# Kernel optimization log

Hardware: AMD Instinct MI355X
Metric: run time of the kernel (lower is better)

Reference implementation:

```python
import jax, jax.numpy as jnp
import numpy as np

B, S, D = 4, 4096, 1024
DFF = 4 * D
ACTIVE = 1024  # ceil(S * 0.25)


def setup_inputs() -> dict:
    key = jax.random.key(0)
    ks = jax.random.split(key, 4)
    x = jax.random.normal(ks[0], (B, S, D), dtype=jnp.float32)
    rw = jax.random.normal(ks[1], (D,), dtype=jnp.float32) * 0.02
    rb = jnp.zeros((1,), dtype=jnp.float32)
    w1 = jax.random.normal(ks[2], (D, DFF), dtype=jnp.float32) * 0.02
    b1 = jnp.zeros((DFF,), dtype=jnp.float32)
    w2 = jax.random.normal(ks[3], (DFF, D), dtype=jnp.float32) * 0.02
    b2 = jnp.zeros((D,), dtype=jnp.float32)
    return {"x": x, "rw": rw, "rb": rb, "w1": w1, "b1": b1,
            "w2": w2, "b2": b2, "active_tokens": ACTIVE}


def reference(x, rw, rb, w1, b1, w2, b2, active_tokens):
    b, s, d = x.shape
    # router: Linear(n_embd, 1) -> [B, S] scores
    scores = jnp.einsum('bsd,d->bs', x, rw) + rb[0]
    # top-k tokens per batch row
    _, idx = jax.lax.top_k(scores, active_tokens)          # [B, K] int32
    sel = jnp.take_along_axis(x, idx[..., None], axis=1)   # [B, K, D]
    # dense MLP on selected tokens (exact GELU as in torch nn.GELU)
    h = jax.nn.gelu(jnp.einsum('bkd,df->bkf', sel, w1) + b1, approximate=False)
    out = jnp.einsum('bkf,fd->bkd', h, w2) + b2            # [B, K, D]
    # sigmoid gate from router scores of selected tokens
    gates = jax.nn.sigmoid(jnp.take_along_axis(scores, idx, axis=1))  # [B, K]
    out = out * gates[..., None]
    # scatter back into zeros at selected positions
    flat_idx = (idx + jnp.arange(b, dtype=idx.dtype)[:, None] * s).reshape(-1)
    flat_out = jnp.zeros((b * s, d), dtype=out.dtype)
    flat_out = flat_out.at[flat_idx].set(out.reshape(-1, d))
    return flat_out.reshape(b, s, d)
```

## Files before the change

### kernel.cpp

```cpp
#include <hip/hip_runtime.h>
#include <hip/hip_bf16.h>
#include <cstdint>
#include <cstddef>

#define Bz 4
#define Sz 4096
#define Dz 1024
#define DFFz 4096
#define KACT 1024

typedef __bf16 bf16;
typedef __attribute__((ext_vector_type(8))) __bf16 bf16x8;
typedef __attribute__((ext_vector_type(4))) __bf16 bf16x4;
typedef __attribute__((ext_vector_type(4))) float f32x4;

__device__ __forceinline__ void async16(const void* g, void* l) {
  __builtin_amdgcn_global_load_lds(
      (const __attribute__((address_space(1))) void*)g,
      (__attribute__((address_space(3))) void*)l, 16, 0, 0);
}

__global__ __launch_bounds__(256) void prep_k(const float* __restrict__ x,
                                              const float* __restrict__ rw,
                                              const float* __restrict__ rb,
                                              float* __restrict__ scores,
                                              float4* __restrict__ out4,
                                              const float* __restrict__ w1,
                                              bf16* __restrict__ w1T,
                                              const float* __restrict__ w2,
                                              bf16* __restrict__ w2T) {
  __shared__ float t[32][33];
  const int bid = blockIdx.x;
  const int tid = threadIdx.x;
  if (bid < 4096) {
    int row = bid * 4 + (tid >> 6);
    int lane = tid & 63;
    const float4* xr = (const float4*)(x + (size_t)row * Dz);
    const float4* wr = (const float4*)rw;
    float acc = 0.f;
#pragma unroll
    for (int i = 0; i < 4; ++i) {
      float4 a = xr[lane + i * 64];
      float4 w = wr[lane + i * 64];
      acc += a.x * w.x + a.y * w.y + a.z * w.z + a.w * w.w;
    }
#pragma unroll
    for (int d = 32; d; d >>= 1) acc += __shfl_down(acc, d, 64);
    if (lane == 0) scores[row] = acc + rb[0];
    float4* o = out4 + (size_t)bid * 4 * (Dz / 4);
    const float4 z = make_float4(0.f, 0.f, 0.f, 0.f);
#pragma unroll
    for (int i = 0; i < 4; ++i) o[tid + i * 256] = z;
  } else {
    const float* in; bf16* outp; int R, C, bx, by;
    if (bid < 8192) {
      in = w1; outp = w1T; R = Dz; C = DFFz;
      bx = (bid - 4096) & 127; by = (bid - 4096) >> 7;
    } else {
      in = w2; outp = w2T; R = DFFz; C = Dz;
      bx = (bid - 8192) & 31; by = (bid - 8192) >> 5;
    }
    int c0 = bx * 32, r0 = by * 32;
    int tx = tid & 31, ty = tid >> 5;
#pragma unroll
    for (int i = 0; i < 32; i += 8) t[ty + i][tx] = in[(size_t)(r0 + ty + i) * C + c0 + tx];
    __syncthreads();
#pragma unroll
    for (int i = 0; i < 32; i += 8)
      outp[(size_t)(c0 + ty + i) * R + r0 + tx] = (bf16)t[tx][ty + i];
  }
}

__global__ __launch_bounds__(256) void select_gather_k(
    const float* __restrict__ x, const float* __restrict__ scores,
    int* __restrict__ sel_idx, float* __restrict__ gates, bf16* __restrict__ Xsel) {
  int b = blockIdx.x >> 8;
  int s0 = (blockIdx.x & 255) * 16;
  __shared__ float sc[Sz];
  __shared__ int red[16][4];
  __shared__ int rk[16];
  const int tid = threadIdx.x;
  const int wave = tid >> 6, lane = tid & 63;
  const float* srow = scores + (size_t)b * Sz;
#pragma unroll
  for (int i = 0; i < 4; ++i)
    ((float4*)sc)[tid + i * 256] = ((const float4*)srow)[tid + i * 256];
  __syncthreads();
  float mine[16];
#pragma unroll
  for (int j = 0; j < 16; ++j) mine[j] = sc[s0 + j];
  int cnt[16] = {};
  for (int t = tid; t < Sz; t += 256) {
    float o = sc[t];
#pragma unroll
    for (int j = 0; j < 16; ++j)
      cnt[j] += (o > mine[j]) || (o == mine[j] && t < s0 + j);
  }
#pragma unroll
  for (int j = 0; j < 16; ++j) {
    int c = cnt[j];
#pragma unroll
    for (int d = 32; d; d >>= 1) c += __shfl_down(c, d, 64);
    if (lane == 0) red[j][wave] = c;
  }
  __syncthreads();
  if (tid < 16) {
    int rank = red[tid][0] + red[tid][1] + red[tid][2] + red[tid][3];
    rk[tid] = rank;
    if (rank < KACT) {
      int m = b * KACT + rank;
      sel_idx[m] = s0 + tid;
      gates[m] = 1.f / (1.f + expf(-sc[s0 + tid]));
    }
  }
  __syncthreads();
#pragma unroll
  for (int j = 0; j < 16; ++j) {
    int rank = rk[j];
    if (rank >= KACT) continue;
    int m = b * KACT + rank;
    float4 v = ((const float4*)(x + ((size_t)b * Sz + s0 + j) * Dz))[tid];
    bf16x4 o = {(bf16)v.x, (bf16)v.y, (bf16)v.z, (bf16)v.w};
    ((bf16x4*)(Xsel + (size_t)m * Dz))[tid] = o;
  }
}


#define BAR_VM0 asm volatile("s_waitcnt vmcnt(0) lgkmcnt(0)\n\ts_barrier" ::: "memory")

#define STG(AS, BS, T)                                                        \
  {                                                                           \
    size_t ko_ = (size_t)(T) * 128;                                           \
    async16(pa0 + ko_, (char*)AS + Ld0);                                      \
    async16(pa1 + ko_, (char*)AS + Ld1);                                      \
    async16(pa2 + ko_, (char*)AS + Ld2);                                      \
    async16(pa3 + ko_, (char*)AS + Ld3);                                      \
    async16(pb0 + ko_, (char*)BS + Ld0);                                      \
    async16(pb1 + ko_, (char*)BS + Ld1);                                      \
    async16(pb2 + ko_, (char*)BS + Ld2);                                      \
    async16(pb3 + ko_, (char*)BS + Ld3);                                      \
  }

#define GB(ARD, BRD, AST, BST, T, DOSTAGE, DOBAR)                             \
  {                                                                           \
    if (DOSTAGE) { STG(AST, BST, (T) + 1) }                                   \
    const char* a_ = (const char*)ARD;                                        \
    const char* b_ = (const char*)BRD;                                        \
    bf16x8 af[2][4], bfr[2][4];                                               \
    _Pragma("unroll") for (int kc = 0; kc < 2; ++kc)                          \
      _Pragma("unroll") for (int i = 0; i < 4; ++i) {                         \
        af[kc][i] = *(const bf16x8*)(a_ + aoff[kc][i]);                       \
        bfr[kc][i] = *(const bf16x8*)(b_ + boff[kc][i]);                      \
      }                                                                       \
    __builtin_amdgcn_s_setprio(1);                                            \
    _Pragma("unroll") for (int kc = 0; kc < 2; ++kc)                          \
      _Pragma("unroll") for (int mi = 0; mi < 4; ++mi)                        \
        _Pragma("unroll") for (int ni = 0; ni < 4; ++ni)                      \
          acc[mi][ni] = __builtin_amdgcn_mfma_f32_16x16x32_bf16(              \
              af[kc][mi], bfr[kc][ni], acc[mi][ni], 0, 0, 0);                 \
    __builtin_amdgcn_s_setprio(0);                                            \
    if (DOBAR) { BAR_VM0; }                                                   \
  }

#define GSETUP(APTR, BPTR, KV, KOFFB)                                         \
  const int tid = threadIdx.x;                                                \
  const int wave = tid >> 6, lane = tid & 63;                                 \
  const int quad = lane >> 4, l16 = lane & 15;                                \
  const int wm = (wave >> 1) * 64, wn = (wave & 1) * 64;                      \
  const int Ld0 = tid * 16, Ld1 = Ld0 + 4096, Ld2 = Ld0 + 8192,               \
            Ld3 = Ld0 + 12288;                                                \
  const int q0 = Ld0 ^ (((Ld0 >> 7) & 7) << 4);                               \
  const int q1 = Ld1 ^ (((Ld1 >> 7) & 7) << 4);                               \
  const int q2 = Ld2 ^ (((Ld2 >> 7) & 7) << 4);                               \
  const int q3 = Ld3 ^ (((Ld3 >> 7) & 7) << 4);                               \
  const char* pa0 = (const char*)(APTR) +                                     \
      ((size_t)(m0 + (q0 >> 7)) * (KV)) * 2 + (KOFFB) + (q0 & 127);           \
  const char* pa1 = (const char*)(APTR) +                                     \
      ((size_t)(m0 + (q1 >> 7)) * (KV)) * 2 + (KOFFB) + (q1 & 127);           \
  const char* pa2 = (const char*)(APTR) +                                     \
      ((size_t)(m0 + (q2 >> 7)) * (KV)) * 2 + (KOFFB) + (q2 & 127);           \
  const char* pa3 = (const char*)(APTR) +                                     \
      ((size_t)(m0 + (q3 >> 7)) * (KV)) * 2 + (KOFFB) + (q3 & 127);           \
  const char* pb0 = (const char*)(BPTR) +                                     \
      ((size_t)(n0 + (q0 >> 7)) * (KV)) * 2 + (KOFFB) + (q0 & 127);           \
  const char* pb1 = (const char*)(BPTR) +                                     \
      ((size_t)(n0 + (q1 >> 7)) * (KV)) * 2 + (KOFFB) + (q1 & 127);           \
  const char* pb2 = (const char*)(BPTR) +                                     \
      ((size_t)(n0 + (q2 >> 7)) * (KV)) * 2 + (KOFFB) + (q2 & 127);           \
  const char* pb3 = (const char*)(BPTR) +                                     \
      ((size_t)(n0 + (q3 >> 7)) * (KV)) * 2 + (KOFFB) + (q3 & 127);           \
  int aoff[2][4], boff[2][4];                                                 \
  _Pragma("unroll") for (int kc = 0; kc < 2; ++kc)                            \
    _Pragma("unroll") for (int i = 0; i < 4; ++i) {                           \
      int ra = wm + i * 16 + l16;                                             \
      int oa = ra * 128 + kc * 64 + quad * 16;                                \
      aoff[kc][i] = oa ^ ((ra & 7) << 4);                                     \
      int rb = wn + i * 16 + l16;                                             \
      int ob = rb * 128 + kc * 64 + quad * 16;                                \
      boff[kc][i] = ob ^ ((rb & 7) << 4);                                     \
    }                                                                         \
  f32x4 acc[4][4] = {};

__global__ __launch_bounds__(256) void gemm1_k(const bf16* __restrict__ A,
                                               const bf16* __restrict__ Bt,
                                               const float* __restrict__ bias,
                                               bf16* __restrict__ H) {
  __shared__ __align__(16) bf16 A0[8192], A1[8192];
  __shared__ __align__(16) bf16 B0[8192], B1[8192];
  const int orig = blockIdx.y * 32 + blockIdx.x;
  const int wgid = (orig & 7) * 128 + (orig >> 3);
  const int m0 = (wgid >> 5) * 128, n0 = (wgid & 31) * 128;
  GSETUP(A, Bt, Dz, 0)
  STG(A0, B0, 0)
  BAR_VM0;
  for (int tt = 0; tt < 7; ++tt) {
    GB(A0, B0, A1, B1, 2 * tt + 0, 1, 1)
    GB(A1, B1, A0, B0, 2 * tt + 1, 1, 1)
  }
  GB(A0, B0, A1, B1, 14, 1, 1)
  GB(A1, B1, A0, B0, 15, 0, 0)
#pragma unroll
  for (int mi = 0; mi < 4; ++mi) {
    int mb = m0 + wm + mi * 16 + quad * 4;
#pragma unroll
    for (int ni = 0; ni < 4; ++ni) {
      int n = n0 + wn + ni * 16 + l16;
      float bn = bias[n];
#pragma unroll
      for (int r = 0; r < 4; ++r) {
        float z = acc[mi][ni][r] + bn;
        float g = 0.5f * z * (1.f + erff(z * 0.70710678118654752f));
        H[(size_t)(mb + r) * DFFz + n] = (bf16)g;
      }
    }
  }
}

__global__ __launch_bounds__(256) void gemm2_k(const bf16* __restrict__ A,
                                               const bf16* __restrict__ Bt,
                                               const float* __restrict__ b2,
                                               const int* __restrict__ sel_idx,
                                               const float* __restrict__ gates,
                                               float* __restrict__ out) {
  __shared__ __align__(16) bf16 A0[8192], A1[8192];
  __shared__ __align__(16) bf16 B0[8192], B1[8192];
  const int orig = blockIdx.y * 8 + blockIdx.x;
  const int wgid = (orig & 7) * 32 + (orig >> 3);
  const int m0 = (wgid >> 3) * 128, n0 = (wgid & 7) * 128;
  GSETUP(A, Bt, DFFz, (size_t)blockIdx.z * 2048 * 2)
  STG(A0, B0, 0)
  BAR_VM0;
  for (int tt = 0; tt < 15; ++tt) {
    GB(A0, B0, A1, B1, 2 * tt + 0, 1, 1)
    GB(A1, B1, A0, B0, 2 * tt + 1, 1, 1)
  }
  GB(A0, B0, A1, B1, 30, 1, 1)
  GB(A1, B1, A0, B0, 31, 0, 0)
  const bool addb = (blockIdx.z == 0);
#pragma unroll
  for (int mi = 0; mi < 4; ++mi) {
#pragma unroll
    for (int r = 0; r < 4; ++r) {
      int m = m0 + wm + mi * 16 + quad * 4 + r;
      int b = m >> 10;
      int s = sel_idx[m];
      float g = gates[m];
      float* orow = out + ((size_t)b * Sz + s) * Dz;
#pragma unroll
      for (int ni = 0; ni < 4; ++ni) {
        int n = n0 + wn + ni * 16 + l16;
        float v = acc[mi][ni][r] + (addb ? b2[n] : 0.f);
        atomicAdd(&orow[n], v * g);
      }
    }
  }
}

extern "C" void kernel_launch(void* const* d_in, const int* in_sizes, int n_in,
                              void* d_out, int out_size, void* d_ws, size_t ws_size,
                              hipStream_t stream) {
  (void)in_sizes; (void)n_in; (void)out_size; (void)ws_size;
  const float* x  = (const float*)d_in[0];
  const float* rw = (const float*)d_in[1];
  const float* rb = (const float*)d_in[2];
  const float* w1 = (const float*)d_in[3];
  const float* b1 = (const float*)d_in[4];
  const float* w2 = (const float*)d_in[5];
  const float* b2 = (const float*)d_in[6];
  float* out = (float*)d_out;

  char* ws = (char*)d_ws;
  float* scores = (float*)ws;  ws += (size_t)Bz * Sz * 4;
  int*   sel_idx = (int*)ws;   ws += (size_t)Bz * KACT * 4;
  float* gates = (float*)ws;   ws += (size_t)Bz * KACT * 4;
  bf16*  w2T = (bf16*)ws;      ws += (size_t)Dz * DFFz * 2;
  bf16*  H = (bf16*)ws;        ws += (size_t)Bz * KACT * DFFz * 2;
  bf16*  w1T = (bf16*)ws;      ws += (size_t)DFFz * Dz * 2;
  bf16*  Xsel = (bf16*)ws;     ws += (size_t)Bz * KACT * Dz * 2;

  prep_k<<<3 * 4096, 256, 0, stream>>>(x, rw, rb, scores, (float4*)out, w1, w1T, w2, w2T);
  select_gather_k<<<Bz * (Sz / 16), 256, 0, stream>>>(x, scores, sel_idx, gates, Xsel);
  gemm1_k<<<dim3(32, 32), 256, 0, stream>>>(Xsel, w1T, b1, H);
  gemm2_k<<<dim3(8, 32, 2), 256, 0, stream>>>(H, w2T, b2, sel_idx, gates, out);
}
```

Measured before the change: 296.3 us.

## Enlarge GEMM tiles to 256x256 with 8 waves and vectorize weight transpose

Both GEMMs move from 128x128 tiles with 4 waves to 256x256 tiles with 8 waves, each wave computing 128x64, to raise data reuse per LDS load. The MFMA inner loop now loads fragments one k-chunk at a time. gemm2 changes its split-K from 2 to 4, with a rotated N offset, which doubles the atomic adds into the output. The weight transpose in prep_k uses 64x64 tiles with float4 loads and 16-byte bf16 stores. The risks are 128KB of LDS per block, which limits occupancy, a grid of only 256 blocks per GEMM, and more atomic traffic.

```diff
diff --git a/kernel.cpp b/kernel.cpp
--- a/kernel.cpp
+++ b/kernel.cpp
@@ -29,7 +29,7 @@
                                               bf16* __restrict__ w1T,
                                               const float* __restrict__ w2,
                                               bf16* __restrict__ w2T) {
-  __shared__ float t[32][33];
+  __shared__ float tt[64][65];
   const int bid = blockIdx.x;
   const int tid = threadIdx.x;
   if (bid < 4096) {
@@ -53,21 +53,32 @@
     for (int i = 0; i < 4; ++i) o[tid + i * 256] = z;
   } else {
     const float* in; bf16* outp; int R, C, bx, by;
-    if (bid < 8192) {
+    if (bid < 5120) {
       in = w1; outp = w1T; R = Dz; C = DFFz;
-      bx = (bid - 4096) & 127; by = (bid - 4096) >> 7;
+      bx = (bid - 4096) & 63; by = (bid - 4096) >> 6;
     } else {
       in = w2; outp = w2T; R = DFFz; C = Dz;
-      bx = (bid - 8192) & 31; by = (bid - 8192) >> 5;
-    }
-    int c0 = bx * 32, r0 = by * 32;
-    int tx = tid & 31, ty = tid >> 5;
-#pragma unroll
-    for (int i = 0; i < 32; i += 8) t[ty + i][tx] = in[(size_t)(r0 + ty + i) * C + c0 + tx];
+      bx = (bid - 5120) & 15; by = (bid - 5120) >> 4;
+    }
+    const int r0 = by * 64, c0 = bx * 64;
+#pragma unroll
+    for (int i = 0; i < 4; ++i) {
+      int row = (tid >> 4) + i * 16;
+      int col = (tid & 15) * 4;
+      float4 v = *(const float4*)&in[(size_t)(r0 + row) * C + c0 + col];
+      tt[row][col] = v.x; tt[row][col + 1] = v.y;
+      tt[row][col + 2] = v.z; tt[row][col + 3] = v.w;
+    }
     __syncthreads();
 #pragma unroll
-    for (int i = 0; i < 32; i += 8)
-      outp[(size_t)(c0 + ty + i) * R + r0 + tx] = (bf16)t[tx][ty + i];
+    for (int i = 0; i < 2; ++i) {
+      int nl = (tid >> 3) + i * 32;
+      int kl = (tid & 7) * 8;
+      bf16x8 o;
+#pragma unroll
+      for (int j = 0; j < 8; ++j) o[j] = (bf16)tt[kl + j][nl];
+      *(bf16x8*)&outp[(size_t)(c0 + nl) * R + r0 + kl] = o;
+    }
   }
 }
 
@@ -146,19 +157,19 @@
     if (DOSTAGE) { STG(AST, BST, (T) + 1) }                                   \
     const char* a_ = (const char*)ARD;                                        \
     const char* b_ = (const char*)BRD;                                        \
-    bf16x8 af[2][4], bfr[2][4];                                               \
-    _Pragma("unroll") for (int kc = 0; kc < 2; ++kc)                          \
-      _Pragma("unroll") for (int i = 0; i < 4; ++i) {                         \
-        af[kc][i] = *(const bf16x8*)(a_ + aoff[kc][i]);                       \
-        bfr[kc][i] = *(const bf16x8*)(b_ + boff[kc][i]);                      \
-      }                                                                       \
-    __builtin_amdgcn_s_setprio(1);                                            \
-    _Pragma("unroll") for (int kc = 0; kc < 2; ++kc)                          \
-      _Pragma("unroll") for (int mi = 0; mi < 4; ++mi)                        \
+    _Pragma("unroll") for (int kc = 0; kc < 2; ++kc) {                        \
+      bf16x8 af[8], bfr[4];                                                   \
+      _Pragma("unroll") for (int i = 0; i < 8; ++i)                           \
+        af[i] = *(const bf16x8*)(a_ + aoff[kc][i]);                           \
+      _Pragma("unroll") for (int i = 0; i < 4; ++i)                           \
+        bfr[i] = *(const bf16x8*)(b_ + boff[kc][i]);                          \
+      __builtin_amdgcn_s_setprio(1);                                          \
+      _Pragma("unroll") for (int mi = 0; mi < 8; ++mi)                        \
         _Pragma("unroll") for (int ni = 0; ni < 4; ++ni)                      \
           acc[mi][ni] = __builtin_amdgcn_mfma_f32_16x16x32_bf16(              \
-              af[kc][mi], bfr[kc][ni], acc[mi][ni], 0, 0, 0);                 \
-    __builtin_amdgcn_s_setprio(0);                                            \
+              af[mi], bfr[ni], acc[mi][ni], 0, 0, 0);                         \
+      __builtin_amdgcn_s_setprio(0);                                          \
+    }                                                                         \
     if (DOBAR) { BAR_VM0; }                                                   \
   }
 
@@ -166,9 +177,9 @@
   const int tid = threadIdx.x;                                                \
   const int wave = tid >> 6, lane = tid & 63;                                 \
   const int quad = lane >> 4, l16 = lane & 15;                                \
-  const int wm = (wave >> 1) * 64, wn = (wave & 1) * 64;                      \
-  const int Ld0 = tid * 16, Ld1 = Ld0 + 4096, Ld2 = Ld0 + 8192,               \
-            Ld3 = Ld0 + 12288;                                                \
+  const int wm = (wave >> 2) * 128, wn = (wave & 3) * 64;                     \
+  const int Ld0 = tid * 16, Ld1 = Ld0 + 8192, Ld2 = Ld0 + 16384,              \
+            Ld3 = Ld0 + 24576;                                                \
   const int q0 = Ld0 ^ (((Ld0 >> 7) & 7) << 4);                               \
   const int q1 = Ld1 ^ (((Ld1 >> 7) & 7) << 4);                               \
   const int q2 = Ld2 ^ (((Ld2 >> 7) & 7) << 4);                               \
@@ -189,27 +200,28 @@
       ((size_t)(n0 + (q2 >> 7)) * (KV)) * 2 + (KOFFB) + (q2 & 127);           \
   const char* pb3 = (const char*)(BPTR) +                                     \
       ((size_t)(n0 + (q3 >> 7)) * (KV)) * 2 + (KOFFB) + (q3 & 127);           \
-  int aoff[2][4], boff[2][4];                                                 \
-  _Pragma("unroll") for (int kc = 0; kc < 2; ++kc)                            \
+  int aoff[2][8], boff[2][4];                                                 \
+  _Pragma("unroll") for (int kc = 0; kc < 2; ++kc) {                          \
+    _Pragma("unroll") for (int i = 0; i < 8; ++i) {                           \
+      int ra = wm + i * 16 + l16;                                             \
+      aoff[kc][i] = (ra * 128 + kc * 64 + quad * 16) ^ ((ra & 7) << 4);       \
+    }                                                                         \
     _Pragma("unroll") for (int i = 0; i < 4; ++i) {                           \
-      int ra = wm + i * 16 + l16;                                             \
-      int oa = ra * 128 + kc * 64 + quad * 16;                                \
-      aoff[kc][i] = oa ^ ((ra & 7) << 4);                                     \
       int rb = wn + i * 16 + l16;                                             \
-      int ob = rb * 128 + kc * 64 + quad * 16;                                \
-      boff[kc][i] = ob ^ ((rb & 7) << 4);                                     \
+      boff[kc][i] = (rb * 128 + kc * 64 + quad * 16) ^ ((rb & 7) << 4);       \
     }                                                                         \
-  f32x4 acc[4][4] = {};
-
-__global__ __launch_bounds__(256) void gemm1_k(const bf16* __restrict__ A,
-                                               const bf16* __restrict__ Bt,
-                                               const float* __restrict__ bias,
-                                               bf16* __restrict__ H) {
-  __shared__ __align__(16) bf16 A0[8192], A1[8192];
-  __shared__ __align__(16) bf16 B0[8192], B1[8192];
-  const int orig = blockIdx.y * 32 + blockIdx.x;
-  const int wgid = (orig & 7) * 128 + (orig >> 3);
-  const int m0 = (wgid >> 5) * 128, n0 = (wgid & 31) * 128;
+  }                                                                           \
+  f32x4 acc[8][4] = {};
+
+__global__ __launch_bounds__(512, 2) void gemm1_k(const bf16* __restrict__ A,
+                                                  const bf16* __restrict__ Bt,
+                                                  const float* __restrict__ bias,
+                                                  bf16* __restrict__ H) {
+  __shared__ __align__(16) bf16 A0[16384], A1[16384];
+  __shared__ __align__(16) bf16 B0[16384], B1[16384];
+  const int orig = blockIdx.y * 16 + blockIdx.x;
+  const int wgid = (orig & 7) * 32 + (orig >> 3);
+  const int m0 = (wgid >> 4) * 256, n0 = (wgid & 15) * 256;
   GSETUP(A, Bt, Dz, 0)
   STG(A0, B0, 0)
   BAR_VM0;
@@ -220,7 +232,7 @@
   GB(A0, B0, A1, B1, 14, 1, 1)
   GB(A1, B1, A0, B0, 15, 0, 0)
 #pragma unroll
-  for (int mi = 0; mi < 4; ++mi) {
+  for (int mi = 0; mi < 8; ++mi) {
     int mb = m0 + wm + mi * 16 + quad * 4;
 #pragma unroll
     for (int ni = 0; ni < 4; ++ni) {
@@ -236,29 +248,30 @@
   }
 }
 
-__global__ __launch_bounds__(256) void gemm2_k(const bf16* __restrict__ A,
-                                               const bf16* __restrict__ Bt,
-                                               const float* __restrict__ b2,
-                                               const int* __restrict__ sel_idx,
-                                               const float* __restrict__ gates,
-                                               float* __restrict__ out) {
-  __shared__ __align__(16) bf16 A0[8192], A1[8192];
-  __shared__ __align__(16) bf16 B0[8192], B1[8192];
-  const int orig = blockIdx.y * 8 + blockIdx.x;
-  const int wgid = (orig & 7) * 32 + (orig >> 3);
-  const int m0 = (wgid >> 3) * 128, n0 = (wgid & 7) * 128;
-  GSETUP(A, Bt, DFFz, (size_t)blockIdx.z * 2048 * 2)
+__global__ __launch_bounds__(512, 2) void gemm2_k(const bf16* __restrict__ A,
+                                                  const bf16* __restrict__ Bt,
+                                                  const float* __restrict__ b2,
+                                                  const int* __restrict__ sel_idx,
+                                                  const float* __restrict__ gates,
+                                                  float* __restrict__ out) {
+  __shared__ __align__(16) bf16 A0[16384], A1[16384];
+  __shared__ __align__(16) bf16 B0[16384], B1[16384];
+  const int orig = blockIdx.y * 4 + blockIdx.x;
+  const int wgid = (orig & 7) * 8 + (orig >> 3);
+  const int m0 = (wgid >> 2) * 256;
+  const int n0 = (((wgid & 3) + blockIdx.z) & 3) * 256;
+  GSETUP(A, Bt, DFFz, (size_t)blockIdx.z * 1024 * 2)
   STG(A0, B0, 0)
   BAR_VM0;
-  for (int tt = 0; tt < 15; ++tt) {
+  for (int tt = 0; tt < 7; ++tt) {
     GB(A0, B0, A1, B1, 2 * tt + 0, 1, 1)
     GB(A1, B1, A0, B0, 2 * tt + 1, 1, 1)
   }
-  GB(A0, B0, A1, B1, 30, 1, 1)
-  GB(A1, B1, A0, B0, 31, 0, 0)
+  GB(A0, B0, A1, B1, 14, 1, 1)
+  GB(A1, B1, A0, B0, 15, 0, 0)
   const bool addb = (blockIdx.z == 0);
 #pragma unroll
-  for (int mi = 0; mi < 4; ++mi) {
+  for (int mi = 0; mi < 8; ++mi) {
 #pragma unroll
     for (int r = 0; r < 4; ++r) {
       int m = m0 + wm + mi * 16 + quad * 4 + r;
@@ -298,8 +311,8 @@
   bf16*  w1T = (bf16*)ws;      ws += (size_t)DFFz * Dz * 2;
   bf16*  Xsel = (bf16*)ws;     ws += (size_t)Bz * KACT * Dz * 2;
 
-  prep_k<<<3 * 4096, 256, 0, stream>>>(x, rw, rb, scores, (float4*)out, w1, w1T, w2, w2T);
+  prep_k<<<6144, 256, 0, stream>>>(x, rw, rb, scores, (float4*)out, w1, w1T, w2, w2T);
   select_gather_k<<<Bz * (Sz / 16), 256, 0, stream>>>(x, scores, sel_idx, gates, Xsel);
-  gemm1_k<<<dim3(32, 32), 256, 0, stream>>>(Xsel, w1T, b1, H);
-  gemm2_k<<<dim3(8, 32, 2), 256, 0, stream>>>(H, w2T, b2, sel_idx, gates, out);
-}
+  gemm1_k<<<dim3(16, 16), 512, 0, stream>>>(Xsel, w1T, b1, H);
+  gemm2_k<<<dim3(4, 16, 4), 512, 0, stream>>>(H, w2T, b2, sel_idx, gates, out);
+}
```

Result: slower. 324.6 us (+9.5%).
